# Kernel tuning notes

Hardware: AMD Instinct MI355X
Metric: run time of the kernel (lower is better)

The kernel has to match this reference:

```python
import jax, jax.numpy as jnp
import numpy as np

B, N, M, C1, C2 = 4, 8192, 2048, 128, 256
H1, H2 = 256, 128  # mlp = [C2+C1, 256, 128]
EPS_DIST = 1e-8
EPS_BN = 1e-5
K = 3


def setup_inputs() -> dict:
    key = jax.random.key(0)
    ks = jax.random.split(key, 6)
    return {
        "unknown": jax.random.normal(ks[0], (B, N, 3), dtype=jnp.float32),
        "known": jax.random.normal(ks[1], (B, M, 3), dtype=jnp.float32),
        "unknow_feats": jax.random.normal(ks[2], (B, C1, N), dtype=jnp.float32),
        "known_feats": jax.random.normal(ks[3], (B, C2, M), dtype=jnp.float32),
        "W1": jax.random.normal(ks[4], (H1, C1 + C2), dtype=jnp.float32) * 0.05,
        "g1": jnp.ones((H1,), jnp.float32),
        "b1": jnp.zeros((H1,), jnp.float32),
        "W2": jax.random.normal(ks[5], (H2, H1), dtype=jnp.float32) * 0.05,
        "g2": jnp.ones((H2,), jnp.float32),
        "b2": jnp.zeros((H2,), jnp.float32),
    }


def _bn_relu(x, g, b):
    # training-mode BatchNorm over (batch, spatial) axes for (B, C, N) tensor
    mean = jnp.mean(x, axis=(0, 2), keepdims=True)
    var = jnp.var(x, axis=(0, 2), keepdims=True)
    y = (x - mean) * jax.lax.rsqrt(var + EPS_BN) * g[None, :, None] + b[None, :, None]
    return jax.nn.relu(y)


def reference(unknown, known, unknow_feats, known_feats, W1, g1, b1, W2, g2, b2):
    # 3-NN: squared euclidean distances (B, N, M) via expansion (avoids B,N,M,3 temp)
    d2 = (
        jnp.sum(unknown * unknown, axis=-1)[:, :, None]
        + jnp.sum(known * known, axis=-1)[:, None, :]
        - 2.0 * jnp.einsum("bnc,bmc->bnm", unknown, known)
    )
    neg_d, idx = jax.lax.top_k(-d2, K)  # smallest-K squared dists
    dist = -neg_d  # (B, N, K), squared distances (pytorch3d knn_points convention)
    recip = 1.0 / (dist + EPS_DIST)
    weight = recip / jnp.sum(recip, axis=2, keepdims=True)  # (B, N, K)

    kf = jnp.swapaxes(known_feats, 1, 2)  # (B, M, C2)
    grouped = jax.vmap(lambda f, i: f[i])(kf, idx)  # (B, N, K, C2)
    interp = jnp.einsum("bnkc,bnk->bcn", grouped, weight)  # (B, C2, N)

    x = jnp.concatenate([interp, unknow_feats], axis=1)  # (B, C2+C1, N)
    x = _bn_relu(jnp.einsum("oc,bcn->bon", W1, x), g1, b1)
    x = _bn_relu(jnp.einsum("oc,bcn->bon", W2, x), g2, b2)
    return x  # (B, H2, N)
```

## Files before the change

### kernel.cpp

```cpp
#include <hip/hip_runtime.h>
#include <hip/hip_bf16.h>
#include <cstdint>
#include <cstddef>

typedef unsigned short u16;
typedef __attribute__((ext_vector_type(8))) short bf16x8;
typedef __attribute__((ext_vector_type(4))) float f32x4;

constexpr int Bn = 4;
constexpr int Nq = 8192;
constexpr int Mk = 2048;
constexpr int C1c = 128;
constexpr int C2c = 256;
constexpr int H1c = 256;
constexpr int H2c = 128;

__device__ __forceinline__ float bf2f(u16 u) {
    union { uint32_t i; float f; } v;
    v.i = (uint32_t)u << 16;
    return v.f;
}
__device__ __forceinline__ u16 f2bf(float f) {
    const uint32_t x = __float_as_uint(f);
    return (u16)((x + 0x7FFFu + ((x >> 16) & 1u)) >> 16);
}

__global__ __launch_bounds__(256) void prep_knn_kernel(
    const float* __restrict__ W1, const float* __restrict__ W2,
    u16* __restrict__ W1b, u16* __restrict__ W2b,
    const float* __restrict__ KF, u16* __restrict__ KFt,
    const float* __restrict__ UF, u16* __restrict__ UFt,
    const float* __restrict__ unknown, const float* __restrict__ known,
    int* __restrict__ idx_out, float* __restrict__ w_out)
{
    __shared__ __align__(16) char smem[32768];
    const int bid = blockIdx.x;
    const int t = threadIdx.x;

    if (bid < 128) {
        const float* X = (bid < 96) ? W1 : W2;
        u16* Y = (bid < 96) ? W1b : W2b;
        const int i = ((bid < 96) ? bid : (bid - 96)) * 256 + t;
        const float4 v = *(const float4*)&X[(size_t)i * 4];
        ushort4 o;
        o.x = f2bf(v.x); o.y = f2bf(v.y); o.z = f2bf(v.z); o.w = f2bf(v.w);
        *(ushort4*)&Y[(size_t)i * 4] = o;
    } else if (bid < 1664) {
        const float* X;
        u16* Y;
        int C, M, m0, c0;
        if (bid < 640) {
            const int f = bid - 128;
            const int b = f >> 7, rem = f & 127;
            C = C2c; M = Mk; m0 = (rem >> 2) * 64; c0 = (rem & 3) * 64;
            X = KF + (size_t)b * C * M;
            Y = KFt + (size_t)b * M * C;
        } else {
            const int f = bid - 640;
            const int b = f >> 8, rem = f & 255;
            C = C1c; M = Nq; m0 = (rem >> 1) * 64; c0 = (rem & 1) * 64;
            X = UF + (size_t)b * C * M;
            Y = UFt + (size_t)b * M * C;
        }
        float (*T)[65] = (float(*)[65])smem;
        const int m4 = (t & 15) * 4, cr = t >> 4;
        #pragma unroll
        for (int i = 0; i < 4; ++i) {
            const float4 v = *(const float4*)&X[(size_t)(c0 + cr + i * 16) * M + m0 + m4];
            T[cr + i * 16][m4 + 0] = v.x;
            T[cr + i * 16][m4 + 1] = v.y;
            T[cr + i * 16][m4 + 2] = v.z;
            T[cr + i * 16][m4 + 3] = v.w;
        }
        __syncthreads();
        const int c4 = (t & 15) * 4, mr = t >> 4;
        #pragma unroll
        for (int i = 0; i < 4; ++i) {
            const int m = mr + i * 16;
            ushort4 o;
            o.x = f2bf(T[c4 + 0][m]);
            o.y = f2bf(T[c4 + 1][m]);
            o.z = f2bf(T[c4 + 2][m]);
            o.w = f2bf(T[c4 + 3][m]);
            *(ushort4*)&Y[(size_t)(m0 + m) * C + c0 + c4] = o;
        }
    } else {
        float4* kp = (float4*)smem;
        const int kbid = bid - 1664;
        const int b = kbid >> 8;
        const int n0 = (kbid & 255) * 32;

        const float* kb = known + (size_t)b * Mk * 3;
        for (int i = t; i < Mk; i += 256) {
            const float x = kb[i * 3 + 0], y = kb[i * 3 + 1], z = kb[i * 3 + 2];
            kp[i] = make_float4(x, y, z, fmaf(x, x, fmaf(y, y, z * z)));
        }
        __syncthreads();

        const int q = n0 + (t >> 3);
        const int s = t & 7;
        const float* u = unknown + ((size_t)b * Nq + q) * 3;
        const float ux = u[0], uy = u[1], uz = u[2];
        const float nux = -2.0f * ux, nuy = -2.0f * uy, nuz = -2.0f * uz;
        const float uu = fmaf(ux, ux, fmaf(uy, uy, uz * uz));

        float d0 = 1e30f, d1 = 1e30f, d2 = 1e30f;
        int i0 = 0, i1 = 0, i2 = 0;
        auto ins = [&](float d, int i) {
            const bool c0 = d < d0, c1 = d < d1, c2 = d < d2;
            d2 = c1 ? d1 : (c2 ? d : d2);
            i2 = c1 ? i1 : (c2 ? i : i2);
            d1 = c0 ? d0 : (c1 ? d : d1);
            i1 = c0 ? i0 : (c1 ? i : i1);
            d0 = c0 ? d : d0;
            i0 = c0 ? i : i0;
        };

        for (int it = 0; it < Mk / 8; ++it) {
            const int m = it * 8 + s;
            const float4 p = kp[m];
            const float d = fmaf(nux, p.x, fmaf(nuy, p.y, fmaf(nuz, p.z, p.w)));
            ins(d, m);
        }
        #pragma unroll
        for (int off = 1; off <= 4; off <<= 1) {
            const float e0 = __shfl_xor(d0, off), e1 = __shfl_xor(d1, off), e2 = __shfl_xor(d2, off);
            const int j0 = __shfl_xor(i0, off), j1 = __shfl_xor(i1, off), j2 = __shfl_xor(i2, off);
            ins(e0, j0);
            ins(e1, j1);
            ins(e2, j2);
        }
        if (s == 0) {
            const float f0 = d0 + uu, f1 = d1 + uu, f2 = d2 + uu;
            const float r0 = 1.0f / (f0 + 1e-8f);
            const float r1 = 1.0f / (f1 + 1e-8f);
            const float r2 = 1.0f / (f2 + 1e-8f);
            const float inv = 1.0f / (r0 + r1 + r2);
            const size_t base = ((size_t)b * Nq + q) * 3;
            idx_out[base + 0] = i0;
            idx_out[base + 1] = i1;
            idx_out[base + 2] = i2;
            w_out[base + 0] = r0 * inv;
            w_out[base + 1] = r1 * inv;
            w_out[base + 2] = r2 * inv;
        }
    }
}

__device__ __forceinline__ uint4 bnx(uint4 x, const float* scs, const float* bis, int k) {
    const u16* p = (const u16*)&x;
    u16 o[8];
    #pragma unroll
    for (int j = 0; j < 8; ++j)
        o[j] = f2bf(fmaxf(0.0f, fmaf(bf2f(p[j]), scs[k + j], bis[k + j])));
    return *(const uint4*)o;
}

template <int GATHER, int OUT_BF16, int STATS, int BNIN>
__global__ __launch_bounds__(256) void mfma_gemm(
    const u16* __restrict__ A, int lda, size_t sA,
    const u16* __restrict__ Bt, int ldb, size_t sB,
    void* __restrict__ Cout, int ldc, size_t sC,
    int nK,
    const u16* __restrict__ Ptb,
    const int* __restrict__ idx, const float* __restrict__ wgt, int nrows,
    const float* __restrict__ bn_s, const float* __restrict__ bn_b,
    float* __restrict__ partS, float* __restrict__ partQ)
{
    __shared__ u16 As[4096];
    __shared__ u16 Bs[4096];
    __shared__ float scs[256], bis[256];
    __shared__ float sS[2][128], sQ[2][128];

    const int b = blockIdx.z;
    const int m0 = blockIdx.x * 128, n0 = blockIdx.y * 128;
    const int t = threadIdx.x;
    const int l = t & 63, wv = t >> 6;
    const int wr = wv >> 1, wc = wv & 1;

    if (BNIN) {
        scs[t] = bn_s[t];
        bis[t] = bn_b[t];
    }

    const u16* Ab = A + (size_t)b * sA;
    const u16* Btb = Bt + (size_t)b * sB;
    const int rA0 = t >> 2, rA1 = (t + 256) >> 2;
    const int ko = (t & 3) * 8;

    f32x4 acc[4][4];
    const f32x4 z = {0.0f, 0.0f, 0.0f, 0.0f};
    #pragma unroll
    for (int i = 0; i < 4; ++i)
        #pragma unroll
        for (int j = 0; j < 4; ++j) acc[i][j] = z;

    uint4 a0 = *(const uint4*)&Ab[(size_t)(m0 + rA0) * lda + ko];
    uint4 a1 = *(const uint4*)&Ab[(size_t)(m0 + rA1) * lda + ko];
    uint4 b0 = *(const uint4*)&Btb[(size_t)(n0 + rA0) * ldb + ko];
    uint4 b1 = *(const uint4*)&Btb[(size_t)(n0 + rA1) * ldb + ko];
    if (BNIN) __syncthreads();

    for (int kt = 0; kt < nK; ++kt) {
        *(uint4*)&As[t * 8] = a0;
        *(uint4*)&As[(t + 256) * 8] = a1;
        if (BNIN) {
            const int k = kt * 32 + ko;
            *(uint4*)&Bs[t * 8] = bnx(b0, scs, bis, k);
            *(uint4*)&Bs[(t + 256) * 8] = bnx(b1, scs, bis, k);
        } else {
            *(uint4*)&Bs[t * 8] = b0;
            *(uint4*)&Bs[(t + 256) * 8] = b1;
        }
        __syncthreads();
        if (kt + 1 < nK) {
            const int k0 = (kt + 1) * 32;
            a0 = *(const uint4*)&Ab[(size_t)(m0 + rA0) * lda + k0 + ko];
            a1 = *(const uint4*)&Ab[(size_t)(m0 + rA1) * lda + k0 + ko];
            b0 = *(const uint4*)&Btb[(size_t)(n0 + rA0) * ldb + k0 + ko];
            b1 = *(const uint4*)&Btb[(size_t)(n0 + rA1) * ldb + k0 + ko];
        }
        bf16x8 af[4], bf[4];
        #pragma unroll
        for (int f = 0; f < 4; ++f) {
            af[f] = *(const bf16x8*)&As[(wr * 64 + f * 16 + (l & 15)) * 32 + (l >> 4) * 8];
            bf[f] = *(const bf16x8*)&Bs[(wc * 64 + f * 16 + (l & 15)) * 32 + (l >> 4) * 8];
        }
        #pragma unroll
        for (int i = 0; i < 4; ++i)
            #pragma unroll
            for (int j = 0; j < 4; ++j)
                acc[i][j] = __builtin_amdgcn_mfma_f32_16x16x32_bf16(af[i], bf[j], acc[i][j], 0, 0, 0);
        __syncthreads();
    }

    const int cb = l & 15;
    const int rg = (l >> 4) * 4;
    float sj[4] = {0, 0, 0, 0}, qj[4] = {0, 0, 0, 0};
    #pragma unroll
    for (int i = 0; i < 4; ++i) {
        #pragma unroll
        for (int r = 0; r < 4; ++r) {
            const int R = m0 + wr * 64 + i * 16 + rg + r;
            const u16 *P0 = nullptr, *P1 = nullptr, *P2 = nullptr;
            float w0 = 0.0f, w1 = 0.0f, w2 = 0.0f;
            if (GATHER) {
                const size_t ib = ((size_t)b * nrows + R) * 3;
                const int j0 = idx[ib], j1 = idx[ib + 1], j2 = idx[ib + 2];
                w0 = wgt[ib];
                w1 = wgt[ib + 1];
                w2 = wgt[ib + 2];
                const u16* Pb = Ptb + (size_t)b * Mk * 256;
                P0 = Pb + (size_t)j0 * 256;
                P1 = Pb + (size_t)j1 * 256;
                P2 = Pb + (size_t)j2 * 256;
            }
            #pragma unroll
            for (int j = 0; j < 4; ++j) {
                const int Cc = n0 + wc * 64 + j * 16 + cb;
                float v = acc[i][j][r];
                if (GATHER)
                    v += w0 * bf2f(P0[Cc]) + w1 * bf2f(P1[Cc]) + w2 * bf2f(P2[Cc]);
                if (OUT_BF16)
                    ((u16*)Cout)[(size_t)b * sC + (size_t)R * ldc + Cc] = f2bf(v);
                else
                    ((float*)Cout)[(size_t)b * sC + (size_t)R * ldc + Cc] = v;
                if (STATS == 1) {
                    sj[j] += v;
                    qj[j] += v * v;
                }
                if (STATS == 2) acc[i][j][r] = v;
            }
        }
    }

    if (STATS == 1) {
        #pragma unroll
        for (int j = 0; j < 4; ++j) {
            float s = sj[j], q = qj[j];
            s += __shfl_xor(s, 16); s += __shfl_xor(s, 32);
            q += __shfl_xor(q, 16); q += __shfl_xor(q, 32);
            if (l < 16) {
                sS[wr][wc * 64 + j * 16 + l] = s;
                sQ[wr][wc * 64 + j * 16 + l] = q;
            }
        }
        __syncthreads();
        if (t < 128) {
            const float S = sS[0][t] + sS[1][t];
            const float Q = sQ[0][t] + sQ[1][t];
            const int pblk = blockIdx.z * gridDim.x + blockIdx.x;
            partS[(size_t)pblk * 256 + blockIdx.y * 128 + t] = S;
            partQ[(size_t)pblk * 256 + blockIdx.y * 128 + t] = Q;
        }
    }
    if (STATS == 2) {
        #pragma unroll
        for (int i = 0; i < 4; ++i) {
            #pragma unroll
            for (int r = 0; r < 4; ++r) {
                float s = acc[i][0][r] + acc[i][1][r] + acc[i][2][r] + acc[i][3][r];
                float q = acc[i][0][r] * acc[i][0][r] + acc[i][1][r] * acc[i][1][r] +
                          acc[i][2][r] * acc[i][2][r] + acc[i][3][r] * acc[i][3][r];
                s += __shfl_xor(s, 1); s += __shfl_xor(s, 2);
                s += __shfl_xor(s, 4); s += __shfl_xor(s, 8);
                q += __shfl_xor(q, 1); q += __shfl_xor(q, 2);
                q += __shfl_xor(q, 4); q += __shfl_xor(q, 8);
                if ((l & 15) == 0) {
                    const int row = wr * 64 + i * 16 + (l >> 4) * 4 + r;
                    sS[wc][row] = s;
                    sQ[wc][row] = q;
                }
            }
        }
        __syncthreads();
        if (t < 128) {
            const float S = sS[0][t] + sS[1][t];
            const float Q = sQ[0][t] + sQ[1][t];
            const int pblk = blockIdx.z * gridDim.y + blockIdx.y;
            partS[(size_t)pblk * 128 + t] = S;
            partQ[(size_t)pblk * 128 + t] = Q;
        }
    }
}

__global__ __launch_bounds__(1024) void bn_finalize(
    const float* __restrict__ pS, const float* __restrict__ pQ,
    const float* __restrict__ g, const float* __restrict__ beta,
    float* __restrict__ scale, float* __restrict__ bias,
    int C, int np, float cnt)
{
    __shared__ float rs[1024], rq[1024];
    const int t = threadIdx.x;
    const int c = t & (C - 1);
    const int sl = t / C;
    const int nsl = 1024 / C;
    float s = 0.0f, q = 0.0f;
    for (int i = sl; i < np; i += nsl) {
        s += pS[(size_t)i * C + c];
        q += pQ[(size_t)i * C + c];
    }
    rs[t] = s;
    rq[t] = q;
    __syncthreads();
    if (t < C) {
        for (int k = 1; k < nsl; ++k) {
            s += rs[t + k * C];
            q += rq[t + k * C];
        }
        const float mean = s / cnt;
        const float var = q / cnt - mean * mean;
        const float r = rsqrtf(var + 1e-5f);
        const float sc = g[t] * r;
        scale[t] = sc;
        bias[t] = beta[t] - mean * sc;
    }
}

__global__ __launch_bounds__(256) void bn2_apply_kernel(
    float* __restrict__ Y,
    const float* __restrict__ pS, const float* __restrict__ pQ,
    const float* __restrict__ g, const float* __restrict__ beta)
{
    __shared__ float rs[256], rq[256];
    const int t = threadIdx.x;
    const size_t base = (size_t)blockIdx.x * 1024;
    const int c = (int)((base / Nq) % H2c);

    rs[t] = pS[(size_t)t * 128 + c];
    rq[t] = pQ[(size_t)t * 128 + c];
    __syncthreads();
    for (int off = 128; off > 0; off >>= 1) {
        if (t < off) {
            rs[t] += rs[t + off];
            rq[t] += rq[t + off];
        }
        __syncthreads();
    }
    if (t == 0) {
        const float cnt = (float)(Bn * Nq);
        const float mean = rs[0] / cnt;
        const float var = rq[0] / cnt - mean * mean;
        const float r = rsqrtf(var + 1e-5f);
        const float sc = g[c] * r;
        rs[0] = sc;
        rq[0] = beta[c] - mean * sc;
    }
    __syncthreads();
    const float sc = rs[0], bi = rq[0];
    float4 v = *(float4*)&Y[base + t * 4];
    v.x = fmaxf(0.0f, fmaf(v.x, sc, bi));
    v.y = fmaxf(0.0f, fmaf(v.y, sc, bi));
    v.z = fmaxf(0.0f, fmaf(v.z, sc, bi));
    v.w = fmaxf(0.0f, fmaf(v.w, sc, bi));
    *(float4*)&Y[base + t * 4] = v;
}

extern "C" void kernel_launch(void* const* d_in, const int* in_sizes, int n_in,
                              void* d_out, int out_size, void* d_ws, size_t ws_size,
                              hipStream_t stream) {
    const float* unknown = (const float*)d_in[0];
    const float* known = (const float*)d_in[1];
    const float* unknow_feats = (const float*)d_in[2];
    const float* known_feats = (const float*)d_in[3];
    const float* W1 = (const float*)d_in[4];
    const float* g1 = (const float*)d_in[5];
    const float* b1 = (const float*)d_in[6];
    const float* W2 = (const float*)d_in[7];
    const float* g2 = (const float*)d_in[8];
    const float* b2 = (const float*)d_in[9];
    float* out = (float*)d_out;

    char* w = (char*)d_ws;
    u16* KFt = (u16*)w; w += (size_t)Bn * Mk * C2c * 2;
    u16* UFt = (u16*)w; w += (size_t)Bn * Nq * C1c * 2;
    u16* W1b = (u16*)w; w += (size_t)H1c * 384 * 2;
    u16* W2b = (u16*)w; w += (size_t)H2c * H1c * 2;
    u16* Ptb = (u16*)w; w += (size_t)Bn * Mk * H1c * 2;
    u16* y1b = (u16*)w; w += (size_t)Bn * Nq * H1c * 2;
    int* idx = (int*)w; w += (size_t)Bn * Nq * 3 * 4;
    float* wgt = (float*)w; w += (size_t)Bn * Nq * 3 * 4;
    float* pS1 = (float*)w; w += (size_t)256 * 256 * 4;
    float* pQ1 = (float*)w; w += (size_t)256 * 256 * 4;
    float* pS2 = (float*)w; w += (size_t)256 * 128 * 4;
    float* pQ2 = (float*)w; w += (size_t)256 * 128 * 4;
    float* scale1 = (float*)w; w += 1024;
    float* bias1 = (float*)w; w += 1024;

    prep_knn_kernel<<<2688, 256, 0, stream>>>(W1, W2, W1b, W2b,
                                              known_feats, KFt, unknow_feats, UFt,
                                              unknown, known, idx, wgt);

    mfma_gemm<0, 1, 0, 0><<<dim3(Mk / 128, H1c / 128, Bn), 256, 0, stream>>>(
        KFt, C2c, (size_t)Mk * C2c,
        W1b, 384, 0,
        Ptb, H1c, (size_t)Mk * H1c,
        C2c / 32, nullptr, nullptr, nullptr, 0,
        nullptr, nullptr, nullptr, nullptr);

    mfma_gemm<1, 1, 1, 0><<<dim3(Nq / 128, H1c / 128, Bn), 256, 0, stream>>>(
        UFt, C1c, (size_t)Nq * C1c,
        W1b + C2c, 384, 0,
        y1b, H1c, (size_t)Nq * H1c,
        C1c / 32, Ptb, idx, wgt, Nq,
        nullptr, nullptr, pS1, pQ1);

    bn_finalize<<<1, 1024, 0, stream>>>(pS1, pQ1, g1, b1, scale1, bias1,
                                        H1c, 256, (float)(Bn * Nq));

    mfma_gemm<0, 0, 2, 1><<<dim3(1, Nq / 128, Bn), 256, 0, stream>>>(
        W2b, H1c, 0,
        y1b, H1c, (size_t)Nq * H1c,
        out, Nq, (size_t)H2c * Nq,
        H1c / 32, nullptr, nullptr, nullptr, 0,
        scale1, bias1, pS2, pQ2);

    bn2_apply_kernel<<<(Bn * H2c * Nq) / 1024, 256, 0, stream>>>(out, pS2, pQ2, g2, b2);
}
```

Before: 109.3 us.

## Split KNN from prep kernel, use med3 top-3 insert, finalize BN2 once

Splits the combined prep/KNN kernel into a dedicated KNN kernel with tighter launch bounds and an unrolled loop, plus a separate transpose/convert kernel. The top-3 insertion now uses fmin/fmed3 for the distances to shorten the select chain. The BN2 statistics reduction, previously redone in every apply block, is computed once by bn_finalize and the apply kernel just reads scale/bias. This removes redundant per-block reductions and shared-memory size coupling, at the cost of two extra kernel launches.

```diff
diff --git a/kernel.cpp b/kernel.cpp
--- a/kernel.cpp
+++ b/kernel.cpp
@@ -25,15 +25,82 @@
     return (u16)((x + 0x7FFFu + ((x >> 16) & 1u)) >> 16);
 }
 
-__global__ __launch_bounds__(256) void prep_knn_kernel(
+__global__ __launch_bounds__(256, 5) void knn_kernel(
+    const float* __restrict__ unknown, const float* __restrict__ known,
+    int* __restrict__ idx_out, float* __restrict__ w_out)
+{
+    __shared__ float4 kp[Mk];
+    const int bid = blockIdx.x;
+    const int t = threadIdx.x;
+    const int b = bid >> 8;
+    const int n0 = (bid & 255) * 32;
+
+    const float* kb = known + (size_t)b * Mk * 3;
+    for (int i = t; i < Mk; i += 256) {
+        const float x = kb[i * 3 + 0], y = kb[i * 3 + 1], z = kb[i * 3 + 2];
+        kp[i] = make_float4(x, y, z, fmaf(x, x, fmaf(y, y, z * z)));
+    }
+    __syncthreads();
+
+    const int q = n0 + (t >> 3);
+    const int s = t & 7;
+    const float* u = unknown + ((size_t)b * Nq + q) * 3;
+    const float ux = u[0], uy = u[1], uz = u[2];
+    const float nux = -2.0f * ux, nuy = -2.0f * uy, nuz = -2.0f * uz;
+    const float uu = fmaf(ux, ux, fmaf(uy, uy, uz * uz));
+
+    float d0 = 1e30f, d1 = 1e30f, d2 = 1e30f;
+    int i0 = 0, i1 = 0, i2 = 0;
+
+    auto ins = [&](float d, int i) {
+        const bool c0 = d < d0, c1 = d < d1, c2 = d < d2;
+        const float nd0 = fminf(d0, d);
+        const float nd1 = __builtin_amdgcn_fmed3f(d0, d, d1);
+        const float nd2 = __builtin_amdgcn_fmed3f(d1, d, d2);
+        i2 = c1 ? i1 : (c2 ? i : i2);
+        i1 = c0 ? i0 : (c1 ? i : i1);
+        i0 = c0 ? i : i0;
+        d0 = nd0; d1 = nd1; d2 = nd2;
+    };
+
+    #pragma unroll 8
+    for (int it = 0; it < Mk / 8; ++it) {
+        const int m = it * 8 + s;
+        const float4 p = kp[m];
+        const float d = fmaf(nux, p.x, fmaf(nuy, p.y, fmaf(nuz, p.z, p.w)));
+        ins(d, m);
+    }
+    #pragma unroll
+    for (int off = 1; off <= 4; off <<= 1) {
+        const float e0 = __shfl_xor(d0, off), e1 = __shfl_xor(d1, off), e2 = __shfl_xor(d2, off);
+        const int j0 = __shfl_xor(i0, off), j1 = __shfl_xor(i1, off), j2 = __shfl_xor(i2, off);
+        ins(e0, j0);
+        ins(e1, j1);
+        ins(e2, j2);
+    }
+    if (s == 0) {
+        const float f0 = d0 + uu, f1 = d1 + uu, f2 = d2 + uu;
+        const float r0 = 1.0f / (f0 + 1e-8f);
+        const float r1 = 1.0f / (f1 + 1e-8f);
+        const float r2 = 1.0f / (f2 + 1e-8f);
+        const float inv = 1.0f / (r0 + r1 + r2);
+        const size_t base = ((size_t)b * Nq + q) * 3;
+        idx_out[base + 0] = i0;
+        idx_out[base + 1] = i1;
+        idx_out[base + 2] = i2;
+        w_out[base + 0] = r0 * inv;
+        w_out[base + 1] = r1 * inv;
+        w_out[base + 2] = r2 * inv;
+    }
+}
+
+__global__ __launch_bounds__(256) void prep_kernel(
     const float* __restrict__ W1, const float* __restrict__ W2,
     u16* __restrict__ W1b, u16* __restrict__ W2b,
     const float* __restrict__ KF, u16* __restrict__ KFt,
-    const float* __restrict__ UF, u16* __restrict__ UFt,
-    const float* __restrict__ unknown, const float* __restrict__ known,
-    int* __restrict__ idx_out, float* __restrict__ w_out)
+    const float* __restrict__ UF, u16* __restrict__ UFt)
 {
-    __shared__ __align__(16) char smem[32768];
+    __shared__ float T[64][65];
     const int bid = blockIdx.x;
     const int t = threadIdx.x;
 
@@ -45,105 +112,44 @@
         ushort4 o;
         o.x = f2bf(v.x); o.y = f2bf(v.y); o.z = f2bf(v.z); o.w = f2bf(v.w);
         *(ushort4*)&Y[(size_t)i * 4] = o;
-    } else if (bid < 1664) {
-        const float* X;
-        u16* Y;
-        int C, M, m0, c0;
-        if (bid < 640) {
-            const int f = bid - 128;
-            const int b = f >> 7, rem = f & 127;
-            C = C2c; M = Mk; m0 = (rem >> 2) * 64; c0 = (rem & 3) * 64;
-            X = KF + (size_t)b * C * M;
-            Y = KFt + (size_t)b * M * C;
-        } else {
-            const int f = bid - 640;
-            const int b = f >> 8, rem = f & 255;
-            C = C1c; M = Nq; m0 = (rem >> 1) * 64; c0 = (rem & 1) * 64;
-            X = UF + (size_t)b * C * M;
-            Y = UFt + (size_t)b * M * C;
-        }
-        float (*T)[65] = (float(*)[65])smem;
-        const int m4 = (t & 15) * 4, cr = t >> 4;
-        #pragma unroll
-        for (int i = 0; i < 4; ++i) {
-            const float4 v = *(const float4*)&X[(size_t)(c0 + cr + i * 16) * M + m0 + m4];
-            T[cr + i * 16][m4 + 0] = v.x;
-            T[cr + i * 16][m4 + 1] = v.y;
-            T[cr + i * 16][m4 + 2] = v.z;
-            T[cr + i * 16][m4 + 3] = v.w;
-        }
-        __syncthreads();
-        const int c4 = (t & 15) * 4, mr = t >> 4;
-        #pragma unroll
-        for (int i = 0; i < 4; ++i) {
-            const int m = mr + i * 16;
-            ushort4 o;
-            o.x = f2bf(T[c4 + 0][m]);
-            o.y = f2bf(T[c4 + 1][m]);
-            o.z = f2bf(T[c4 + 2][m]);
-            o.w = f2bf(T[c4 + 3][m]);
-            *(ushort4*)&Y[(size_t)(m0 + m) * C + c0 + c4] = o;
-        }
+        return;
+    }
+    const float* X;
+    u16* Y;
+    int C, M, m0, c0;
+    if (bid < 640) {
+        const int f = bid - 128;
+        const int b = f >> 7, rem = f & 127;
+        C = C2c; M = Mk; m0 = (rem >> 2) * 64; c0 = (rem & 3) * 64;
+        X = KF + (size_t)b * C * M;
+        Y = KFt + (size_t)b * M * C;
     } else {
-        float4* kp = (float4*)smem;
-        const int kbid = bid - 1664;
-        const int b = kbid >> 8;
-        const int n0 = (kbid & 255) * 32;
-
-        const float* kb = known + (size_t)b * Mk * 3;
-        for (int i = t; i < Mk; i += 256) {
-            const float x = kb[i * 3 + 0], y = kb[i * 3 + 1], z = kb[i * 3 + 2];
-            kp[i] = make_float4(x, y, z, fmaf(x, x, fmaf(y, y, z * z)));
-        }
-        __syncthreads();
-
-        const int q = n0 + (t >> 3);
-        const int s = t & 7;
-        const float* u = unknown + ((size_t)b * Nq + q) * 3;
-        const float ux = u[0], uy = u[1], uz = u[2];
-        const float nux = -2.0f * ux, nuy = -2.0f * uy, nuz = -2.0f * uz;
-        const float uu = fmaf(ux, ux, fmaf(uy, uy, uz * uz));
-
-        float d0 = 1e30f, d1 = 1e30f, d2 = 1e30f;
-        int i0 = 0, i1 = 0, i2 = 0;
-        auto ins = [&](float d, int i) {
-            const bool c0 = d < d0, c1 = d < d1, c2 = d < d2;
-            d2 = c1 ? d1 : (c2 ? d : d2);
-            i2 = c1 ? i1 : (c2 ? i : i2);
-            d1 = c0 ? d0 : (c1 ? d : d1);
-            i1 = c0 ? i0 : (c1 ? i : i1);
-            d0 = c0 ? d : d0;
-            i0 = c0 ? i : i0;
-        };
-
-        for (int it = 0; it < Mk / 8; ++it) {
-            const int m = it * 8 + s;
-            const float4 p = kp[m];
-            const float d = fmaf(nux, p.x, fmaf(nuy, p.y, fmaf(nuz, p.z, p.w)));
-            ins(d, m);
-        }
-        #pragma unroll
-        for (int off = 1; off <= 4; off <<= 1) {
-            const float e0 = __shfl_xor(d0, off), e1 = __shfl_xor(d1, off), e2 = __shfl_xor(d2, off);
-            const int j0 = __shfl_xor(i0, off), j1 = __shfl_xor(i1, off), j2 = __shfl_xor(i2, off);
-            ins(e0, j0);
-            ins(e1, j1);
-            ins(e2, j2);
-        }
-        if (s == 0) {
-            const float f0 = d0 + uu, f1 = d1 + uu, f2 = d2 + uu;
-            const float r0 = 1.0f / (f0 + 1e-8f);
-            const float r1 = 1.0f / (f1 + 1e-8f);
-            const float r2 = 1.0f / (f2 + 1e-8f);
-            const float inv = 1.0f / (r0 + r1 + r2);
-            const size_t base = ((size_t)b * Nq + q) * 3;
-            idx_out[base + 0] = i0;
-            idx_out[base + 1] = i1;
-            idx_out[base + 2] = i2;
-            w_out[base + 0] = r0 * inv;
-            w_out[base + 1] = r1 * inv;
-            w_out[base + 2] = r2 * inv;
-        }
+        const int f = bid - 640;
+        const int b = f >> 8, rem = f & 255;
+        C = C1c; M = Nq; m0 = (rem >> 1) * 64; c0 = (rem & 1) * 64;
+        X = UF + (size_t)b * C * M;
+        Y = UFt + (size_t)b * M * C;
+    }
+    const int m4 = (t & 15) * 4, cr = t >> 4;
+    #pragma unroll
+    for (int i = 0; i < 4; ++i) {
+        const float4 v = *(const float4*)&X[(size_t)(c0 + cr + i * 16) * M + m0 + m4];
+        T[cr + i * 16][m4 + 0] = v.x;
+        T[cr + i * 16][m4 + 1] = v.y;
+        T[cr + i * 16][m4 + 2] = v.z;
+        T[cr + i * 16][m4 + 3] = v.w;
+    }
+    __syncthreads();
+    const int c4 = (t & 15) * 4, mr = t >> 4;
+    #pragma unroll
+    for (int i = 0; i < 4; ++i) {
+        const int m = mr + i * 16;
+        ushort4 o;
+        o.x = f2bf(T[c4 + 0][m]);
+        o.y = f2bf(T[c4 + 1][m]);
+        o.z = f2bf(T[c4 + 2][m]);
+        o.w = f2bf(T[c4 + 3][m]);
+        *(ushort4*)&Y[(size_t)(m0 + m) * C + c0 + c4] = o;
     }
 }
 
@@ -357,43 +363,19 @@
     }
 }
 
-__global__ __launch_bounds__(256) void bn2_apply_kernel(
-    float* __restrict__ Y,
-    const float* __restrict__ pS, const float* __restrict__ pQ,
-    const float* __restrict__ g, const float* __restrict__ beta)
+__global__ __launch_bounds__(256) void bn2_apply_simple(
+    float* __restrict__ Y, const float* __restrict__ scale, const float* __restrict__ bias)
 {
-    __shared__ float rs[256], rq[256];
-    const int t = threadIdx.x;
     const size_t base = (size_t)blockIdx.x * 1024;
     const int c = (int)((base / Nq) % H2c);
-
-    rs[t] = pS[(size_t)t * 128 + c];
-    rq[t] = pQ[(size_t)t * 128 + c];
-    __syncthreads();
-    for (int off = 128; off > 0; off >>= 1) {
-        if (t < off) {
-            rs[t] += rs[t + off];
-            rq[t] += rq[t + off];
-        }
-        __syncthreads();
-    }
-    if (t == 0) {
-        const float cnt = (float)(Bn * Nq);
-        const float mean = rs[0] / cnt;
-        const float var = rq[0] / cnt - mean * mean;
-        const float r = rsqrtf(var + 1e-5f);
-        const float sc = g[c] * r;
-        rs[0] = sc;
-        rq[0] = beta[c] - mean * sc;
-    }
-    __syncthreads();
-    const float sc = rs[0], bi = rq[0];
-    float4 v = *(float4*)&Y[base + t * 4];
+    const float sc = scale[c], bi = bias[c];
+    const size_t i = base + threadIdx.x * 4;
+    float4 v = *(float4*)&Y[i];
     v.x = fmaxf(0.0f, fmaf(v.x, sc, bi));
     v.y = fmaxf(0.0f, fmaf(v.y, sc, bi));
     v.z = fmaxf(0.0f, fmaf(v.z, sc, bi));
     v.w = fmaxf(0.0f, fmaf(v.w, sc, bi));
-    *(float4*)&Y[base + t * 4] = v;
+    *(float4*)&Y[i] = v;
 }
 
 extern "C" void kernel_launch(void* const* d_in, const int* in_sizes, int n_in,
@@ -426,10 +408,13 @@
     float* pQ2 = (float*)w; w += (size_t)256 * 128 * 4;
     float* scale1 = (float*)w; w += 1024;
     float* bias1 = (float*)w; w += 1024;
-
-    prep_knn_kernel<<<2688, 256, 0, stream>>>(W1, W2, W1b, W2b,
-                                              known_feats, KFt, unknow_feats, UFt,
-                                              unknown, known, idx, wgt);
+    float* scale2 = (float*)w; w += 1024;
+    float* bias2 = (float*)w; w += 1024;
+
+    knn_kernel<<<1024, 256, 0, stream>>>(unknown, known, idx, wgt);
+
+    prep_kernel<<<1664, 256, 0, stream>>>(W1, W2, W1b, W2b,
+                                          known_feats, KFt, unknow_feats, UFt);
 
     mfma_gemm<0, 1, 0, 0><<<dim3(Mk / 128, H1c / 128, Bn), 256, 0, stream>>>(
         KFt, C2c, (size_t)Mk * C2c,
@@ -455,5 +440,8 @@
         H1c / 32, nullptr, nullptr, nullptr, 0,
         scale1, bias1, pS2, pQ2);
 
-    bn2_apply_kernel<<<(Bn * H2c * Nq) / 1024, 256, 0, stream>>>(out, pS2, pQ2, g2, b2);
-}
+    bn_finalize<<<1, 1024, 0, stream>>>(pS2, pQ2, g2, b2, scale2, bias2,
+                                        H2c, 256, (float)(Bn * Nq));
+
+    bn2_apply_simple<<<(Bn * H2c * Nq) / 1024, 256, 0, stream>>>(out, scale2, bias2);
+}
```

Measured after the change: 117.2 us. +7.3%, slower.
